# Optimization experiments

Hardware: AMD Instinct MI355X
Metric: run time of the kernel (lower is better)

The kernel has to match this reference:

```python
import jax, jax.numpy as jnp
import numpy as np

NUM_HEADS = 16
MODEL_DIM = 1024
DEPTH = MODEL_DIM // NUM_HEADS
B, S = 4, 1024


def setup_inputs() -> dict:
    key = jax.random.key(0)
    ks = jax.random.split(key, 12)
    sc = 1.0 / np.sqrt(MODEL_DIM)
    q = jax.random.normal(ks[0], (B, S, MODEL_DIM), jnp.float32)
    k = jax.random.normal(ks[1], (B, S, MODEL_DIM), jnp.float32)
    v = jax.random.normal(ks[2], (B, S, MODEL_DIM), jnp.float32)
    # binary padding mask, 1 = masked position (added as mask * -1e9)
    mask = (jax.random.uniform(ks[3], (B, 1, 1, S)) < 0.1).astype(jnp.float32)
    Wq = jax.random.normal(ks[4], (MODEL_DIM, MODEL_DIM), jnp.float32) * sc
    bq = jnp.zeros((MODEL_DIM,), jnp.float32)
    Wk = jax.random.normal(ks[5], (MODEL_DIM, MODEL_DIM), jnp.float32) * sc
    bk = jnp.zeros((MODEL_DIM,), jnp.float32)
    Wv = jax.random.normal(ks[6], (MODEL_DIM, MODEL_DIM), jnp.float32) * sc
    bv = jnp.zeros((MODEL_DIM,), jnp.float32)
    Wo = jax.random.normal(ks[7], (MODEL_DIM, MODEL_DIM), jnp.float32) * sc
    bo = jnp.zeros((MODEL_DIM,), jnp.float32)
    return dict(q=q, k=k, v=v, mask=mask, Wq=Wq, bq=bq, Wk=Wk, bk=bk,
                Wv=Wv, bv=bv, Wo=Wo, bo=bo)


def _split_head(x):
    b, s, _ = x.shape
    return x.reshape(b, s, NUM_HEADS, DEPTH).transpose(0, 2, 1, 3)


def reference(q, k, v, mask, Wq, bq, Wk, bk, Wv, bv, Wo, bo):
    Q = _split_head(q @ Wq + bq)   # (B,H,S,depth)
    K = _split_head(k @ Wk + bk)
    V = _split_head(v @ Wv + bv)
    # NOTE: original divides by k_dim (depth), NOT sqrt(depth) -- keep faithful
    logits = jnp.einsum('bhqd,bhkd->bhqk', Q, K) / jnp.float32(DEPTH)
    logits = logits + mask * (-1e9)
    attn = jax.nn.softmax(logits, axis=-1)         # (B,H,Sq,Sk)
    ctx = jnp.einsum('bhqk,bhkd->bhqd', attn, V)   # (B,H,S,depth)
    ctx = ctx.transpose(0, 2, 1, 3).reshape(q.shape[0], -1, MODEL_DIM)
    out = ctx @ Wo + bo
    return out, attn
```

## Files before the change

### kernel.cpp

```cpp
#include <hip/hip_runtime.h>
#include <stdint.h>
#include <stddef.h>

#define DEV __device__ __forceinline__

typedef __bf16 bf16_t;
typedef bf16_t bf16x8 __attribute__((ext_vector_type(8)));
typedef float f32x4 __attribute__((ext_vector_type(4)));
typedef unsigned short us4 __attribute__((ext_vector_type(4)));
typedef unsigned short us8 __attribute__((ext_vector_type(8)));

DEV float bf2f(unsigned short u) {
    union { unsigned int i; float f; } w; w.i = ((unsigned int)u) << 16; return w.f;
}
DEV unsigned short f2bf(float f) {
    union { unsigned int i; float f; } w; w.f = f;
    unsigned int u = w.i;
    return (unsigned short)((u + 0x7fffu + ((u >> 16) & 1u)) >> 16);
}

DEV void gl_lds16(const void* g, void* l) {
    __builtin_amdgcn_global_load_lds((const __attribute__((address_space(1))) void*)g,
                                     (__attribute__((address_space(3))) void*)l,
                                     16, 0, 0);
}

__global__ void __launch_bounds__(256)
cvt3(const float* __restrict__ s0, const float* __restrict__ s1, const float* __restrict__ s2,
     unsigned short* __restrict__ d0, unsigned short* __restrict__ d1, unsigned short* __restrict__ d2) {
    const float* src    = (blockIdx.z == 0) ? s0 : (blockIdx.z == 1) ? s1 : s2;
    unsigned short* dst = (blockIdx.z == 0) ? d0 : (blockIdx.z == 1) ? d1 : d2;
    int idx = (blockIdx.x * 256 + threadIdx.x) * 4;
    f32x4 v = *(const f32x4*)&src[idx];
    us4 o;
#pragma unroll
    for (int i = 0; i < 4; i++) o[i] = f2bf(v[i]);
    *(us4*)&dst[idx] = o;
}

__global__ void __launch_bounds__(256)
transpose_w(const float* __restrict__ W0, const float* __restrict__ W1,
            const float* __restrict__ W2, const float* __restrict__ W3,
            unsigned short* __restrict__ T0, unsigned short* __restrict__ T1,
            unsigned short* __restrict__ T2, unsigned short* __restrict__ T3) {
    const float* W    = (blockIdx.z == 0) ? W0 : (blockIdx.z == 1) ? W1 : (blockIdx.z == 2) ? W2 : W3;
    unsigned short* T = (blockIdx.z == 0) ? T0 : (blockIdx.z == 1) ? T1 : (blockIdx.z == 2) ? T2 : T3;
    __shared__ float t[32][33];
    int tx = threadIdx.x, ty = threadIdx.y;
    int k0 = blockIdx.x * 32, n0 = blockIdx.y * 32;
#pragma unroll
    for (int r = 0; r < 4; r++)
        t[ty + r * 8][tx] = W[(size_t)(k0 + ty + r * 8) * 1024 + n0 + tx];
    __syncthreads();
#pragma unroll
    for (int r = 0; r < 4; r++)
        T[(size_t)(n0 + ty + r * 8) * 1024 + k0 + tx] = f2bf(t[tx][ty + r * 8]);
}

__global__ void __launch_bounds__(256)
qkv_gemm(const unsigned short* __restrict__ Aq, const unsigned short* __restrict__ Ak,
         const unsigned short* __restrict__ Av,
         const unsigned short* __restrict__ BtQ, const unsigned short* __restrict__ BtK,
         const unsigned short* __restrict__ BtV,
         const float* __restrict__ biq, const float* __restrict__ bik,
         const float* __restrict__ biv,
         unsigned short* __restrict__ Qw, unsigned short* __restrict__ Kw,
         unsigned short* __restrict__ Vtw) {
    const int K = 1024;
    const unsigned short* A  = (blockIdx.z == 0) ? Aq  : (blockIdx.z == 1) ? Ak  : Av;
    const unsigned short* Bt = (blockIdx.z == 0) ? BtQ : (blockIdx.z == 1) ? BtK : BtV;
    const float* bias        = (blockIdx.z == 0) ? biq : (blockIdx.z == 1) ? bik : biv;
    unsigned short* Cout     = (blockIdx.z == 0) ? Qw  : (blockIdx.z == 1) ? Kw  : Vtw;
    const bool vmode = (blockIdx.z == 2);

    __shared__ __align__(16) unsigned short As[128 * 32];
    __shared__ __align__(16) unsigned short Bs[128 * 32];
    int tid = threadIdx.x, lane = tid & 63, wid = tid >> 6;
    int mBase = blockIdx.x * 128, nBase = blockIdx.y * 128;
    int wm = (wid >> 1) * 64, wn = (wid & 1) * 64;
    int c0 = lane & 15, quad = lane >> 4;

    f32x4 acc[4][4] = {};

    for (int k0 = 0; k0 < K; k0 += 32) {
        __syncthreads();
#pragma unroll
        for (int i = 0; i < 2; i++) {
            int cb = wid * 64 + 256 * i;
            int cc = cb + lane;
            int row = cc >> 2, kc = cc & 3;
            gl_lds16(A  + (size_t)(mBase + row) * K + k0 + kc * 8, &As[cb * 8]);
            gl_lds16(Bt + (size_t)(nBase + row) * K + k0 + kc * 8, &Bs[cb * 8]);
        }
        __syncthreads();
        bf16x8 af[4], bfr[4];
#pragma unroll
        for (int t = 0; t < 4; t++) {
            af[t]  = *(const bf16x8*)&As[(wm + t * 16 + c0) * 32 + quad * 8];
            bfr[t] = *(const bf16x8*)&Bs[(wn + t * 16 + c0) * 32 + quad * 8];
        }
#pragma unroll
        for (int mt = 0; mt < 4; mt++)
#pragma unroll
            for (int nt = 0; nt < 4; nt++)
                acc[mt][nt] = __builtin_amdgcn_mfma_f32_16x16x32_bf16(af[mt], bfr[nt], acc[mt][nt], 0, 0, 0);
    }

#pragma unroll
    for (int mt = 0; mt < 4; mt++) {
#pragma unroll
        for (int nt = 0; nt < 4; nt++) {
            int n = nBase + wn + nt * 16 + c0;
            float bv = bias[n];
            if (vmode) {
                int m0 = mBase + wm + mt * 16 + quad * 4;
                int b = m0 >> 10, s = m0 & 1023, h = n >> 6, d = n & 63;
                us4 pk;
#pragma unroll
                for (int r = 0; r < 4; r++) pk[r] = f2bf(acc[mt][nt][r] + bv);
                *(us4*)&Cout[((size_t)((b * 16 + h) * 64 + d)) * 1024 + s] = pk;
            } else {
#pragma unroll
                for (int r = 0; r < 4; r++) {
                    int m = mBase + wm + mt * 16 + quad * 4 + r;
                    int b = m >> 10, s = m & 1023, h = n >> 6, d = n & 63;
                    Cout[((size_t)((b * 16 + h) * 1024 + s)) * 64 + d] = f2bf(acc[mt][nt][r] + bv);
                }
            }
        }
    }
}

__global__ void __launch_bounds__(256)
out_gemm(const unsigned short* __restrict__ A,
         const unsigned short* __restrict__ Bt,
         const float* __restrict__ bias,
         float* __restrict__ Cout) {
    const int K = 1024;
    __shared__ __align__(16) unsigned short As[128 * 32];
    __shared__ __align__(16) unsigned short Bs[128 * 32];
    int tid = threadIdx.x, lane = tid & 63, wid = tid >> 6;
    int mBase = blockIdx.x * 128, nBase = blockIdx.y * 128;
    int wm = (wid >> 1) * 64, wn = (wid & 1) * 64;
    int c0 = lane & 15, quad = lane >> 4;

    f32x4 acc[4][4] = {};

    for (int k0 = 0; k0 < K; k0 += 32) {
        __syncthreads();
#pragma unroll
        for (int i = 0; i < 2; i++) {
            int cb = wid * 64 + 256 * i;
            int cc = cb + lane;
            int row = cc >> 2, kc = cc & 3;
            gl_lds16(A  + (size_t)(mBase + row) * K + k0 + kc * 8, &As[cb * 8]);
            gl_lds16(Bt + (size_t)(nBase + row) * K + k0 + kc * 8, &Bs[cb * 8]);
        }
        __syncthreads();
        bf16x8 af[4], bfr[4];
#pragma unroll
        for (int t = 0; t < 4; t++) {
            af[t]  = *(const bf16x8*)&As[(wm + t * 16 + c0) * 32 + quad * 8];
            bfr[t] = *(const bf16x8*)&Bs[(wn + t * 16 + c0) * 32 + quad * 8];
        }
#pragma unroll
        for (int mt = 0; mt < 4; mt++)
#pragma unroll
            for (int nt = 0; nt < 4; nt++)
                acc[mt][nt] = __builtin_amdgcn_mfma_f32_16x16x32_bf16(af[mt], bfr[nt], acc[mt][nt], 0, 0, 0);
    }
#pragma unroll
    for (int mt = 0; mt < 4; mt++)
#pragma unroll
        for (int nt = 0; nt < 4; nt++) {
            int n = nBase + wn + nt * 16 + c0;
            float bv = bias[n];
#pragma unroll
            for (int r = 0; r < 4; r++) {
                int m = mBase + wm + mt * 16 + quad * 4 + r;
                Cout[(size_t)m * 1024 + n] = acc[mt][nt][r] + bv;
            }
        }
}

__global__ void __launch_bounds__(256)
attn_pv(const unsigned short* __restrict__ Qws,
        const unsigned short* __restrict__ Kws,
        const unsigned short* __restrict__ Vtw,
        const float* __restrict__ maskp,
        float* __restrict__ attnOut,
        unsigned short* __restrict__ ctx) {
    __shared__ __align__(16) unsigned short ldsA[17408];
    __shared__ __align__(16) unsigned short Vs[17408];
    __shared__ float redbuf[4][16];

    int tid = threadIdx.x, lane = tid & 63, wid = tid >> 6;
    int c0 = lane & 15, quad = lane >> 4;
    int bh = blockIdx.y, b = bh >> 4, h = bh & 15;
    int q0 = blockIdx.x * 16;

    bf16x8 aq0, aq1;
    {
        const unsigned short* qp = Qws + ((size_t)bh * 1024 + q0 + c0) * 64 + quad * 8;
        aq0 = *(const bf16x8*)qp;
        aq1 = *(const bf16x8*)(qp + 32);
    }

    f32x4 acc[16] = {};

    for (int ch = 0; ch < 4; ch++) {
        __syncthreads();
#pragma unroll
        for (int i = 0; i < 8; i++) {
            int cb = wid * 64 + 256 * i;
            int cc = cb + lane;
            int row = cc >> 3, kc = cc & 7;
            gl_lds16(Kws + ((size_t)bh * 1024 + ch * 256 + row) * 64 + kc * 8, &ldsA[cb * 8]);
        }
        __syncthreads();
#pragma unroll
        for (int nt = 0; nt < 4; nt++) {
            int srow = wid * 64 + nt * 16 + c0;
            const unsigned short* kp = &ldsA[srow * 64 + quad * 8];
            bf16x8 b0 = *(const bf16x8*)kp;
            bf16x8 b1 = *(const bf16x8*)(kp + 32);
            int ai = ch * 4 + nt;
            acc[ai] = __builtin_amdgcn_mfma_f32_16x16x32_bf16(aq0, b0, acc[ai], 0, 0, 0);
            acc[ai] = __builtin_amdgcn_mfma_f32_16x16x32_bf16(aq1, b1, acc[ai], 0, 0, 0);
        }
    }

    float lmax[4] = {-3e38f, -3e38f, -3e38f, -3e38f};
#pragma unroll
    for (int i = 0; i < 16; i++) {
        int col = (i >> 2) * 256 + wid * 64 + (i & 3) * 16 + c0;
        float mval = maskp[b * 1024 + col] * (-1e9f);
#pragma unroll
        for (int r = 0; r < 4; r++) {
            float v = acc[i][r] * (1.0f / 64.0f) + mval;
            acc[i][r] = v;
            lmax[r] = fmaxf(lmax[r], v);
        }
    }
#pragma unroll
    for (int st = 1; st < 16; st <<= 1) {
#pragma unroll
        for (int r = 0; r < 4; r++) lmax[r] = fmaxf(lmax[r], __shfl_xor(lmax[r], st, 64));
    }
    if (c0 == 0) {
#pragma unroll
        for (int r = 0; r < 4; r++) redbuf[wid][quad * 4 + r] = lmax[r];
    }
    __syncthreads();
    float rmax[4];
#pragma unroll
    for (int r = 0; r < 4; r++) {
        int row = quad * 4 + r;
        rmax[r] = fmaxf(fmaxf(redbuf[0][row], redbuf[1][row]), fmaxf(redbuf[2][row], redbuf[3][row]));
    }
    float lsum[4] = {0.f, 0.f, 0.f, 0.f};
#pragma unroll
    for (int i = 0; i < 16; i++) {
#pragma unroll
        for (int r = 0; r < 4; r++) {
            float e = __expf(acc[i][r] - rmax[r]);
            acc[i][r] = e;
            lsum[r] += e;
        }
    }
#pragma unroll
    for (int st = 1; st < 16; st <<= 1) {
#pragma unroll
        for (int r = 0; r < 4; r++) lsum[r] += __shfl_xor(lsum[r], st, 64);
    }
    __syncthreads();
    if (c0 == 0) {
#pragma unroll
        for (int r = 0; r < 4; r++) redbuf[wid][quad * 4 + r] = lsum[r];
    }
    __syncthreads();
    float rinv[4];
#pragma unroll
    for (int r = 0; r < 4; r++) {
        int row = quad * 4 + r;
        rinv[r] = 1.0f / (redbuf[0][row] + redbuf[1][row] + redbuf[2][row] + redbuf[3][row]);
    }

    size_t gbase = ((size_t)bh * 1024 + q0) * 1024;
#pragma unroll
    for (int i = 0; i < 16; i++) {
        int kk = (i >> 2) * 64 + (i & 3) * 16 + c0;
        int col = (i >> 2) * 256 + wid * 64 + (i & 3) * 16 + c0;
        int kks = kk ^ (quad << 3);
#pragma unroll
        for (int r = 0; r < 4; r++) {
            int row = quad * 4 + r;
            float pv = acc[i][r] * rinv[r];
            attnOut[gbase + (size_t)row * 1024 + col] = pv;
            ldsA[wid * 4352 + row * 272 + kks] = f2bf(pv);
        }
    }

    f32x4 ctxacc = {};
    for (int ch = 0; ch < 4; ch++) {
        __syncthreads();
#pragma unroll
        for (int i = 0; i < 8; i++) {
            int cidx = tid + 256 * i;
            int drow = cidx >> 5;
            int soff = (cidx & 31) * 8;
            us8 val = *(const us8*)&Vtw[((size_t)(bh * 64 + drow)) * 1024 + ch * 256 + soff];
            *(us8*)&Vs[drow * 272 + soff] = val;
        }
        __syncthreads();
#pragma unroll
        for (int wv = 0; wv < 4; wv++) {
#pragma unroll
            for (int t = 0; t < 2; t++) {
                int kidx = (ch * 64 + t * 32 + quad * 8) ^ ((c0 >> 2) << 3);
                bf16x8 a  = *(const bf16x8*)&ldsA[wv * 4352 + c0 * 272 + kidx];
                bf16x8 bf_ = *(const bf16x8*)&Vs[(wid * 16 + c0) * 272 + wv * 64 + t * 32 + quad * 8];
                ctxacc = __builtin_amdgcn_mfma_f32_16x16x32_bf16(a, bf_, ctxacc, 0, 0, 0);
            }
        }
    }
#pragma unroll
    for (int r = 0; r < 4; r++) {
        int s = q0 + quad * 4 + r;
        ctx[((size_t)(b * 1024 + s)) * 1024 + h * 64 + wid * 16 + c0] = f2bf(ctxacc[r]);
    }
}

extern "C" void kernel_launch(void* const* d_in, const int* in_sizes, int n_in,
                              void* d_out, int out_size, void* d_ws, size_t ws_size,
                              hipStream_t stream) {
    (void)in_sizes; (void)n_in; (void)out_size; (void)ws_size;
    const float* q    = (const float*)d_in[0];
    const float* k    = (const float*)d_in[1];
    const float* v    = (const float*)d_in[2];
    const float* mask = (const float*)d_in[3];
    const float* Wq   = (const float*)d_in[4];
    const float* bq   = (const float*)d_in[5];
    const float* Wk   = (const float*)d_in[6];
    const float* bk   = (const float*)d_in[7];
    const float* Wv   = (const float*)d_in[8];
    const float* bv   = (const float*)d_in[9];
    const float* Wo   = (const float*)d_in[10];
    const float* bo   = (const float*)d_in[11];

    float* outF  = (float*)d_out;
    float* attnF = outF + (size_t)4 * 1024 * 1024;

    unsigned short* wsu = (unsigned short*)d_ws;
    const size_t M1 = (size_t)1024 * 1024;
    unsigned short* WqT = wsu + 0 * M1;
    unsigned short* WkT = wsu + 1 * M1;
    unsigned short* WvT = wsu + 2 * M1;
    unsigned short* WoT = wsu + 3 * M1;
    unsigned short* tq  = wsu + 4 * M1;
    unsigned short* tk  = wsu + 8 * M1;
    unsigned short* tv  = wsu + 12 * M1;
    unsigned short* Qw  = wsu + 16 * M1;
    unsigned short* Kw  = wsu + 20 * M1;
    unsigned short* Vtw = wsu + 24 * M1;
    unsigned short* ctx = wsu + 28 * M1;

    transpose_w<<<dim3(32, 32, 4), dim3(32, 8), 0, stream>>>(Wq, Wk, Wv, Wo, WqT, WkT, WvT, WoT);

    cvt3<<<dim3(4096, 1, 3), 256, 0, stream>>>(q, k, v, tq, tk, tv);

    qkv_gemm<<<dim3(32, 8, 3), 256, 0, stream>>>(tq, tk, tv, WqT, WkT, WvT, bq, bk, bv, Qw, Kw, Vtw);

    attn_pv<<<dim3(64, 64), 256, 0, stream>>>(Qw, Kw, Vtw, mask, attnF, ctx);

    out_gemm<<<dim3(32, 8), 256, 0, stream>>>(ctx, WoT, bo, outF);
}
```

Baseline: 497.1 us.

## Load K and V fragments directly from global memory in attention kernel

The attention kernel no longer stages K and V tiles through shared memory. Each wave reads its MFMA operands straight from global memory, which removes most __syncthreads barriers and halves LDS usage so more blocks can be resident (launch bounds now request 3 per SIMD). The attention probabilities are written with nontemporal stores, and the PV accumulation is split into two independent accumulators to expose more MFMA parallelism. The cost is uncoalesced, cache-dependent global loads and possible register pressure under the tighter occupancy bound.

After: 521.9 us. +5.0%, slower.

```diff
diff --git a/kernel.cpp b/kernel.cpp
--- a/kernel.cpp
+++ b/kernel.cpp
@@ -183,15 +183,14 @@
         }
 }
 
-__global__ void __launch_bounds__(256)
+__global__ void __launch_bounds__(256, 3)
 attn_pv(const unsigned short* __restrict__ Qws,
         const unsigned short* __restrict__ Kws,
         const unsigned short* __restrict__ Vtw,
         const float* __restrict__ maskp,
         float* __restrict__ attnOut,
         unsigned short* __restrict__ ctx) {
-    __shared__ __align__(16) unsigned short ldsA[17408];
-    __shared__ __align__(16) unsigned short Vs[17408];
+    __shared__ __align__(16) unsigned short ldsP[17408];
     __shared__ float redbuf[4][16];
 
     int tid = threadIdx.x, lane = tid & 63, wid = tid >> 6;
@@ -208,20 +207,13 @@
 
     f32x4 acc[16] = {};
 
+    const unsigned short* kbase = Kws + (size_t)bh * 1024 * 64;
+#pragma unroll
     for (int ch = 0; ch < 4; ch++) {
-        __syncthreads();
-#pragma unroll
-        for (int i = 0; i < 8; i++) {
-            int cb = wid * 64 + 256 * i;
-            int cc = cb + lane;
-            int row = cc >> 3, kc = cc & 7;
-            gl_lds16(Kws + ((size_t)bh * 1024 + ch * 256 + row) * 64 + kc * 8, &ldsA[cb * 8]);
-        }
-        __syncthreads();
 #pragma unroll
         for (int nt = 0; nt < 4; nt++) {
-            int srow = wid * 64 + nt * 16 + c0;
-            const unsigned short* kp = &ldsA[srow * 64 + quad * 8];
+            int srow = ch * 256 + wid * 64 + nt * 16 + c0;
+            const unsigned short* kp = kbase + (size_t)srow * 64 + quad * 8;
             bf16x8 b0 = *(const bf16x8*)kp;
             bf16x8 b1 = *(const bf16x8*)(kp + 32);
             int ai = ch * 4 + nt;
@@ -296,34 +288,30 @@
         for (int r = 0; r < 4; r++) {
             int row = quad * 4 + r;
             float pv = acc[i][r] * rinv[r];
-            attnOut[gbase + (size_t)row * 1024 + col] = pv;
-            ldsA[wid * 4352 + row * 272 + kks] = f2bf(pv);
-        }
-    }
-
-    f32x4 ctxacc = {};
+            __builtin_nontemporal_store(pv, &attnOut[gbase + (size_t)row * 1024 + col]);
+            ldsP[wid * 4352 + row * 272 + kks] = f2bf(pv);
+        }
+    }
+    __syncthreads();
+
+    f32x4 ctx0 = {}, ctx1 = {};
+    const unsigned short* vbase = Vtw + ((size_t)(bh * 64 + wid * 16 + c0)) * 1024 + quad * 8;
+#pragma unroll
     for (int ch = 0; ch < 4; ch++) {
-        __syncthreads();
-#pragma unroll
-        for (int i = 0; i < 8; i++) {
-            int cidx = tid + 256 * i;
-            int drow = cidx >> 5;
-            int soff = (cidx & 31) * 8;
-            us8 val = *(const us8*)&Vtw[((size_t)(bh * 64 + drow)) * 1024 + ch * 256 + soff];
-            *(us8*)&Vs[drow * 272 + soff] = val;
-        }
-        __syncthreads();
 #pragma unroll
         for (int wv = 0; wv < 4; wv++) {
-#pragma unroll
-            for (int t = 0; t < 2; t++) {
-                int kidx = (ch * 64 + t * 32 + quad * 8) ^ ((c0 >> 2) << 3);
-                bf16x8 a  = *(const bf16x8*)&ldsA[wv * 4352 + c0 * 272 + kidx];
-                bf16x8 bf_ = *(const bf16x8*)&Vs[(wid * 16 + c0) * 272 + wv * 64 + t * 32 + quad * 8];
-                ctxacc = __builtin_amdgcn_mfma_f32_16x16x32_bf16(a, bf_, ctxacc, 0, 0, 0);
-            }
-        }
-    }
+            int kidx0 = (ch * 64 + quad * 8) ^ ((c0 >> 2) << 3);
+            int kidx1 = (ch * 64 + 32 + quad * 8) ^ ((c0 >> 2) << 3);
+            bf16x8 a0 = *(const bf16x8*)&ldsP[wv * 4352 + c0 * 272 + kidx0];
+            bf16x8 a1 = *(const bf16x8*)&ldsP[wv * 4352 + c0 * 272 + kidx1];
+            bf16x8 v0 = *(const bf16x8*)&vbase[ch * 256 + wv * 64];
+            bf16x8 v1 = *(const bf16x8*)&vbase[ch * 256 + wv * 64 + 32];
+            ctx0 = __builtin_amdgcn_mfma_f32_16x16x32_bf16(a0, v0, ctx0, 0, 0, 0);
+            ctx1 = __builtin_amdgcn_mfma_f32_16x16x32_bf16(a1, v1, ctx1, 0, 0, 0);
+        }
+    }
+    f32x4 ctxacc = ctx0 + ctx1;
+
 #pragma unroll
     for (int r = 0; r < 4; r++) {
         int s = q0 + quad * 4 + r;
```
